# Kernel tuning notes

Measured on AMD Instinct MI355X. Metric: run time of the kernel, lower is better.

## Reference

```python
import jax, jax.numpy as jnp
import numpy as np

L, B, D = 512, 16, 256
H = 4            # MAX_DIFF == num_heads
MAX_BONDS = 6
MAX_DIFF = 4
PROB_SHIFT = 0.3


def _attn_weights(x, Wqk, Wq, bq, Wk, bk, mask):
    """Per-head softmax(QK^T/sqrt(hd)) with key padding mask.
    x: [b,l,d]; Wqk: [d,2d] (the inc/dec_qk pre-projection);
    Wq/Wk: [d,d] (MHA in_proj, stored x@W layout); mask: [b,l] bool (True=masked).
    Returns [b,h,l,l]. The V path / out_proj of the torch MHA are discarded
    by the original module, so they are omitted here.
    """
    b, l, d = x.shape
    hd = d // H
    q = x @ Wqk[:, :d]
    k = x @ Wqk[:, d:]
    Q = (q @ Wq + bq).reshape(b, l, H, hd)
    K = (k @ Wk + bk).reshape(b, l, H, hd)
    scores = jnp.einsum('blhd,bmhd->bhlm', Q, K) / np.sqrt(hd)
    scores = jnp.where(mask[:, None, None, :], -jnp.inf, scores)
    return jax.nn.softmax(scores, axis=-1)


def setup_inputs() -> dict:
    key = jax.random.key(0)
    ks = jax.random.split(key, 16)
    s = 0.05
    p = lambda k, shape: jax.random.normal(k, shape, jnp.float32) * s
    # key_padding_mask: last 64 positions padded (True == masked)
    src_mask = jnp.broadcast_to(jnp.arange(L)[None, :] >= (L - 64), (B, L))
    return {
        'molecule_embedding': jax.random.normal(ks[0], (L, B, D), jnp.float32),
        'src_bond': jax.random.randint(ks[1], (B, L, MAX_BONDS), 0, L, jnp.int32),
        'src_mask': src_mask,
        'W_inc_qk': p(ks[2], (D, 2 * D)),
        'Wq_inc': p(ks[3], (D, D)), 'bq_inc': p(ks[4], (D,)),
        'Wk_inc': p(ks[5], (D, D)), 'bk_inc': p(ks[6], (D,)),
        'W_dec_qk': p(ks[7], (D, 2 * D)),
        'Wq_dec': p(ks[8], (D, D)), 'bq_dec': p(ks[9], (D,)),
        'Wk_dec': p(ks[10], (D, D)), 'bk_dec': p(ks[11], (D,)),
        'Wc': p(ks[12], (MAX_DIFF, MAX_DIFF)), 'bc': p(ks[13], (MAX_DIFF,)),
    }


def reference(molecule_embedding, src_bond, src_mask,
              W_inc_qk, Wq_inc, bq_inc, Wk_inc, bk_inc,
              W_dec_qk, Wq_dec, bq_dec, Wk_dec, bk_dec,
              Wc, bc):
    x = jnp.transpose(molecule_embedding, (1, 0, 2))  # [b,l,d]
    b, l, _ = x.shape

    inc = _attn_weights(x, W_inc_qk, Wq_inc, bq_inc, Wk_inc, bk_inc, src_mask)
    dec = _attn_weights(x, W_dec_qk, Wq_dec, bq_dec, Wk_dec, bk_dec, src_mask)

    pad = (~src_mask).astype(jnp.float32)              # 1 - mask
    pm2 = pad[:, :, None] * pad[:, None, :]            # [b,l,l]

    # cls_layer((inc-dec).permute(0,2,3,1)) * (MAX_DIFF*pad_mask)[...,None]
    diff = (jnp.einsum('bhlm,hc->blmc', inc - dec, Wc) + bc)
    diff = diff * (MAX_DIFF * pm2)[..., None]          # [b,l,l,4]

    # src_bond has last dim == MAX_BONDS -> one-hot neighbor counts
    src_w = jax.nn.one_hot(src_bond, l, dtype=jnp.float32).sum(axis=2) * pm2  # [b,l,l]
    eye = jnp.eye(l, dtype=jnp.float32)
    src_w = src_w * (1.0 - eye)[None]                  # zero diagonal

    # _shift_probs(src_weight.long(), prob_shift, MAX_DIFF)
    oh = jax.nn.one_hot(src_w.astype(jnp.int32), MAX_DIFF, dtype=jnp.float32)
    probs = oh * (1.0 - PROB_SHIFT) + (1.0 - oh) * (PROB_SHIFT / (MAX_DIFF - 1))
    probs = probs / probs.sum(axis=-1, keepdims=True)

    return jnp.log(probs + 1e-6) + diff                # [b,l,l,4]
```

## Files before the change

kernel.cpp:

```cpp
#include <hip/hip_runtime.h>
#include <stdint.h>

typedef unsigned short u16t;
typedef short s8v __attribute__((ext_vector_type(8)));
typedef float f4v __attribute__((ext_vector_type(4)));

#define MFMA16 __builtin_amdgcn_mfma_f32_16x16x32_bf16
#define QKN (16*4*512*64)

__device__ __forceinline__ u16t f2bf(float f) {
  unsigned u = __builtin_bit_cast(unsigned, f);
  u += 0x7fffu + ((u >> 16) & 1u);
  return (u16t)(u >> 16);
}

__global__ __launch_bounds__(256) void prep_kernel(
    const float* __restrict__ Wiqk, const float* __restrict__ Wqi, const float* __restrict__ Wki,
    const float* __restrict__ Wdqk, const float* __restrict__ Wqd, const float* __restrict__ Wkd,
    u16t* __restrict__ weffT, const int* __restrict__ mraw, int* __restrict__ mdst) {
  __shared__ float At[16][65];
  __shared__ float Bt[16][65];
  __shared__ int mode;
  const int tid = threadIdx.x;

  if (blockIdx.z == 4) {
    if (tid == 0) mode = 0;
    __syncthreads();
    unsigned v0 = (unsigned)mraw[tid], v1 = (unsigned)mraw[tid + 256];
    if (v0 == 0x3F800000u || v1 == 0x3F800000u) mode = 2;
    __syncthreads();
    if (mode == 0 && (v0 > 1u || v1 > 1u)) mode = 1;
    __syncthreads();
    const int g = blockIdx.y * 4 + blockIdx.x;
#pragma unroll
    for (int i = 0; i < 2; ++i) {
      int idx = g * 512 + i * 256 + tid;
      int m;
      if (mode == 2)      m = (((const float*)mraw)[idx] != 0.0f) ? 1 : 0;
      else if (mode == 1) m = ((const unsigned char*)mraw)[idx];
      else                m = mraw[idx];
      mdst[idx] = m;
    }
    return;
  }

  const int n0 = blockIdx.x * 64;
  const int d0 = blockIdx.y * 64;
  const int p  = blockIdx.z;
  const float* A2  = (p == 0) ? Wqi : (p == 1) ? Wki : (p == 2) ? Wqd : Wkd;
  const float* Wqk = (p < 2) ? Wiqk : Wdqk;
  const int aoff = (p & 1) * 256;
  const int tx = tid & 15, ty = tid >> 4;

  float acc[4][4];
#pragma unroll
  for (int i = 0; i < 4; ++i)
#pragma unroll
    for (int j = 0; j < 4; ++j) acc[i][j] = 0.f;

  for (int k0 = 0; k0 < 256; k0 += 16) {
    __syncthreads();
    {
      int nn = tid & 63, kr = tid >> 6;
#pragma unroll
      for (int pass = 0; pass < 4; ++pass) {
        int kk = kr + pass * 4;
        At[kk][nn] = A2[(size_t)(k0 + kk) * 256 + n0 + nn];
      }
      int kk = tid & 15, dr = tid >> 4;
#pragma unroll
      for (int pass = 0; pass < 4; ++pass) {
        int dd = dr + pass * 16;
        Bt[kk][dd] = Wqk[(size_t)(d0 + dd) * 512 + aoff + k0 + kk];
      }
    }
    __syncthreads();
#pragma unroll
    for (int kk = 0; kk < 16; ++kk) {
      float a[4], b[4];
#pragma unroll
      for (int i = 0; i < 4; ++i) a[i] = At[kk][ty * 4 + i];
#pragma unroll
      for (int j = 0; j < 4; ++j) b[j] = Bt[kk][tx * 4 + j];
#pragma unroll
      for (int i = 0; i < 4; ++i)
#pragma unroll
        for (int j = 0; j < 4; ++j) acc[i][j] = fmaf(a[i], b[j], acc[i][j]);
    }
  }

#pragma unroll
  for (int i = 0; i < 4; ++i) {
    u16t h[4] = {f2bf(acc[i][0]), f2bf(acc[i][1]), f2bf(acc[i][2]), f2bf(acc[i][3])};
    *(uint2*)(&weffT[((size_t)(p * 256 + n0 + ty * 4 + i)) * 256 + d0 + tx * 4]) =
        *(const uint2*)h;
  }
}

__global__ __launch_bounds__(256) void proj_kernel(
    const float* __restrict__ emb, const u16t* __restrict__ weffT,
    const float* __restrict__ bq_inc, const float* __restrict__ bk_inc,
    const float* __restrict__ bq_dec, const float* __restrict__ bk_dec,
    u16t* __restrict__ qk) {
  __shared__ __align__(16) u16t As[128 * 40];
  __shared__ __align__(16) u16t Bs[128 * 40];
  const int t = threadIdx.x;
  const int n0 = blockIdx.x * 128;
  const int r0 = blockIdx.y * 128;
  const int bb = r0 >> 9;
  const int l0 = r0 & 511;
  const int lane = t & 63, wid = t >> 6;
  const int quad = lane >> 4, c15 = lane & 15;
  const int wm = wid >> 1, wn = wid & 1;

  f4v acc[4][4];
#pragma unroll
  for (int i = 0; i < 4; ++i)
#pragma unroll
    for (int j = 0; j < 4; ++j) acc[i][j] = f4v{0.f, 0.f, 0.f, 0.f};

  for (int k0 = 0; k0 < 256; k0 += 32) {
    __syncthreads();
#pragma unroll
    for (int i = 0; i < 2; ++i) {
      int c = t + i * 256;
      int m = c >> 2, off = (c & 3) * 8;
      const float* src = emb + (size_t)((l0 + m) * 16 + bb) * 256 + k0 + off;
      float4 x0 = *(const float4*)src;
      float4 x1 = *(const float4*)(src + 4);
      u16t h[8] = {f2bf(x0.x), f2bf(x0.y), f2bf(x0.z), f2bf(x0.w),
                   f2bf(x1.x), f2bf(x1.y), f2bf(x1.z), f2bf(x1.w)};
      *(uint4*)(&As[m * 40 + off]) = *(const uint4*)h;
      *(uint4*)(&Bs[m * 40 + off]) =
          *(const uint4*)(weffT + (size_t)(n0 + m) * 256 + k0 + off);
    }
    __syncthreads();
    s8v af[4], bf[4];
#pragma unroll
    for (int mi = 0; mi < 4; ++mi)
      af[mi] = *(const s8v*)(&As[(wm * 64 + mi * 16 + c15) * 40 + quad * 8]);
#pragma unroll
    for (int ni = 0; ni < 4; ++ni)
      bf[ni] = *(const s8v*)(&Bs[(wn * 64 + ni * 16 + c15) * 40 + quad * 8]);
#pragma unroll
    for (int mi = 0; mi < 4; ++mi)
#pragma unroll
      for (int ni = 0; ni < 4; ++ni)
        acc[mi][ni] = MFMA16(af[mi], bf[ni], acc[mi][ni], 0, 0, 0);
  }

  const float* biasP[4] = {bq_inc, bk_inc, bq_dec, bk_dec};
#pragma unroll
  for (int ni = 0; ni < 4; ++ni) {
    int n = n0 + wn * 64 + ni * 16 + c15;
    int p = n >> 8, h = (n >> 6) & 3, tt = n & 63, jj = n & 255;
    float bias = biasP[p][jj];
    u16t* dst = qk + (size_t)p * QKN;
#pragma unroll
    for (int mi = 0; mi < 4; ++mi) {
#pragma unroll
      for (int reg = 0; reg < 4; ++reg) {
        int l = l0 + wm * 64 + mi * 16 + quad * 4 + reg;
        dst[((size_t)(bb * 4 + h) * 512 + l) * 64 + tt] = f2bf(acc[mi][ni][reg] + bias);
      }
    }
  }
}

__global__ __launch_bounds__(512) void fused_kernel(
    const u16t* __restrict__ qk, const int* __restrict__ mask,
    const int* __restrict__ src_bond, const float* __restrict__ Wc,
    const float* __restrict__ bc, float* __restrict__ out) {
  __shared__ __align__(16) u16t Qs[8 * 16 * 72];
  __shared__ int bondsL[96];
  __shared__ int mlds[512 + 16];
  __shared__ float rpart[2][8][16];
  const int t = threadIdx.x;
  const int l0 = blockIdx.x * 16;
  const int bb = blockIdx.y;

#pragma unroll
  for (int i = 0; i < 2; ++i) {
    int c = t + i * 512;
    int q = c >> 7, row = (c >> 3) & 15, off = (c & 7) * 8;
    const u16t* Qb = qk + (size_t)(2 * (q >> 2)) * QKN;
    *(uint4*)(&Qs[(q * 16 + row) * 72 + off]) =
        *(const uint4*)(Qb + ((size_t)(bb * 4 + (q & 3)) * 512 + l0 + row) * 64 + off);
  }
  mlds[t] = mask[bb * 512 + t];
  if (t < 16) mlds[512 + t] = mask[bb * 512 + l0 + t];
  if (t < 96) bondsL[t] = src_bond[(size_t)(bb * 512 + l0 + t / 6) * 6 + (t % 6)];

  const int lane = t & 63, wid = t >> 6;
  const int quad = lane >> 4, c15 = lane & 15;

  float Wf[16];
#pragma unroll
  for (int i = 0; i < 16; ++i) Wf[i] = Wc[i];

  float dacc[4][4][4];
#pragma unroll
  for (int nt = 0; nt < 4; ++nt)
#pragma unroll
    for (int r = 0; r < 4; ++r)
#pragma unroll
      for (int c = 0; c < 4; ++c) dacc[nt][r][c] = 0.f;

  __syncthreads();

#pragma unroll 1
  for (int q = 0; q < 8; ++q) {
    const int pp = q >> 2, h = q & 3;
    const u16t* Kb = qk + (size_t)(2 * pp + 1) * QKN + (size_t)(bb * 4 + h) * 512 * 64;
    s8v a0 = *(const s8v*)(&Qs[(q * 16 + c15) * 72 + quad * 8]);
    s8v a1 = *(const s8v*)(&Qs[(q * 16 + c15) * 72 + 32 + quad * 8]);

    s8v kb0[4], kb1[4];
#pragma unroll
    for (int nt = 0; nt < 4; ++nt) {
      int m = wid * 64 + nt * 16 + c15;
      kb0[nt] = *(const s8v*)(Kb + (size_t)m * 64 + quad * 8);
      kb1[nt] = *(const s8v*)(Kb + (size_t)m * 64 + 32 + quad * 8);
    }

    float E[4][4];
    float rsum[4] = {0.f, 0.f, 0.f, 0.f};
#pragma unroll
    for (int nt = 0; nt < 4; ++nt) {
      f4v sacc = f4v{0.f, 0.f, 0.f, 0.f};
      sacc = MFMA16(a0, kb0[nt], sacc, 0, 0, 0);
      sacc = MFMA16(a1, kb1[nt], sacc, 0, 0, 0);
      int m = wid * 64 + nt * 16 + c15;
      bool msk = (mlds[m] != 0);
#pragma unroll
      for (int reg = 0; reg < 4; ++reg) {
        float e = msk ? 0.f : __expf(sacc[reg] * 0.125f);
        E[nt][reg] = e;
        rsum[reg] += e;
      }
    }

#pragma unroll
    for (int reg = 0; reg < 4; ++reg) {
#pragma unroll
      for (int off = 1; off < 16; off <<= 1) rsum[reg] += __shfl_xor(rsum[reg], off);
    }
    if (c15 == 0) {
#pragma unroll
      for (int reg = 0; reg < 4; ++reg) rpart[q & 1][wid][quad * 4 + reg] = rsum[reg];
    }
    __syncthreads();

    float inv[4];
    const float sgn = pp ? -1.f : 1.f;
#pragma unroll
    for (int reg = 0; reg < 4; ++reg) {
      float tot = 0.f;
#pragma unroll
      for (int w = 0; w < 8; ++w) tot += rpart[q & 1][w][quad * 4 + reg];
      inv[reg] = sgn / tot;
    }

#pragma unroll
    for (int nt = 0; nt < 4; ++nt) {
#pragma unroll
      for (int reg = 0; reg < 4; ++reg) {
        float P = E[nt][reg] * inv[reg];
#pragma unroll
        for (int c = 0; c < 4; ++c)
          dacc[nt][reg][c] = fmaf(P, Wf[h * 4 + c], dacc[nt][reg][c]);
      }
    }
  }

  float bcF[4];
#pragma unroll
  for (int c = 0; c < 4; ++c) bcF[c] = bc[c];
  const float lgH = logf(0.7f + 1e-6f);
  const float lgM = logf(0.1f + 1e-6f);
  const float lgU = logf(0.25f + 1e-6f);

#pragma unroll
  for (int nt = 0; nt < 4; ++nt) {
    int m = wid * 64 + nt * 16 + c15;
    bool padm = (mlds[m] == 0);
#pragma unroll
    for (int reg = 0; reg < 4; ++reg) {
      int lloc = quad * 4 + reg;
      int l = l0 + lloc;
      bool padl = (mlds[512 + lloc] == 0);
      bool pm = padl && padm;
      int cnt = 0;
#pragma unroll
      for (int j = 0; j < 6; ++j) cnt += (bondsL[lloc * 6 + j] == m) ? 1 : 0;
      int cls = (pm && (m != l)) ? cnt : 0;
      float v[4];
#pragma unroll
      for (int c = 0; c < 4; ++c) {
        float lp = (cls >= 4) ? lgU : ((c == cls) ? lgH : lgM);
        float dv = pm ? 4.f * (dacc[nt][reg][c] + bcF[c]) : 0.f;
        v[c] = lp + dv;
      }
      float4 o = make_float4(v[0], v[1], v[2], v[3]);
      *(float4*)(&out[((size_t)(bb * 512 + l) * 512 + m) * 4]) = o;
    }
  }
}

extern "C" void kernel_launch(void* const* d_in, const int* in_sizes, int n_in,
                              void* d_out, int out_size, void* d_ws, size_t ws_size,
                              hipStream_t stream) {
  (void)in_sizes; (void)n_in; (void)out_size; (void)ws_size;
  const float* emb      = (const float*)d_in[0];
  const int*   src_bond = (const int*)d_in[1];
  const int*   mask_raw = (const int*)d_in[2];
  const float* W_inc_qk = (const float*)d_in[3];
  const float* Wq_inc   = (const float*)d_in[4];
  const float* bq_inc   = (const float*)d_in[5];
  const float* Wk_inc   = (const float*)d_in[6];
  const float* bk_inc   = (const float*)d_in[7];
  const float* W_dec_qk = (const float*)d_in[8];
  const float* Wq_dec   = (const float*)d_in[9];
  const float* bq_dec   = (const float*)d_in[10];
  const float* Wk_dec   = (const float*)d_in[11];
  const float* bk_dec   = (const float*)d_in[12];
  const float* Wc       = (const float*)d_in[13];
  const float* bc       = (const float*)d_in[14];
  float* out = (float*)d_out;

  char* ws = (char*)d_ws;
  int*   wsMask = (int*)ws;
  u16t*  weffT  = (u16t*)(ws + 32768);
  u16t*  qk     = (u16t*)(ws + 32768 + 524288);

  hipLaunchKernelGGL(prep_kernel, dim3(4, 4, 5), dim3(256), 0, stream,
                     W_inc_qk, Wq_inc, Wk_inc, W_dec_qk, Wq_dec, Wk_dec, weffT,
                     mask_raw, wsMask);
  hipLaunchKernelGGL(proj_kernel, dim3(8, 64), dim3(256), 0, stream,
                     emb, weffT, bq_inc, bk_inc, bq_dec, bk_dec, qk);
  hipLaunchKernelGGL(fused_kernel, dim3(32, 16), dim3(512), 0, stream,
                     qk, wsMask, src_bond, Wc, bc, out);
}
```

Before: 195.2 us.

## Prefetch next head's K tiles, remap blocks across batches, move Wc to LDS

The K fragments for the next head are loaded into registers while the current head's softmax reduction and accumulation run, so global load latency overlaps with compute instead of stalling each iteration. Block indices are remapped so that neighbouring workgroups cover different batches, which spreads K reads across batches and XCDs. Wc is staged through LDS rather than held as 16 registers, the key mask is hoisted out of the loop, and the partial-sum layout is transposed so each row total is read with two float4 loads. The prefetch raises register pressure because K is live across the barrier, and the block remap assumes a 32x16 grid.

```diff
diff --git a/kernel.cpp b/kernel.cpp
--- a/kernel.cpp
+++ b/kernel.cpp
@@ -174,10 +174,14 @@
   __shared__ __align__(16) u16t Qs[8 * 16 * 72];
   __shared__ int bondsL[96];
   __shared__ int mlds[512 + 16];
-  __shared__ float rpart[2][8][16];
+  __shared__ __align__(16) float rpart[2][16][8];
+  __shared__ float wlds[16];
   const int t = threadIdx.x;
-  const int l0 = blockIdx.x * 16;
-  const int bb = blockIdx.y;
+
+  const int f = (int)(blockIdx.x + gridDim.x * blockIdx.y);
+  const int j = f >> 3;
+  const int bb = (f & 7) * 2 + (j >> 5);
+  const int l0 = (j & 31) * 16;
 
 #pragma unroll
   for (int i = 0; i < 2; ++i) {
@@ -190,13 +194,11 @@
   mlds[t] = mask[bb * 512 + t];
   if (t < 16) mlds[512 + t] = mask[bb * 512 + l0 + t];
   if (t < 96) bondsL[t] = src_bond[(size_t)(bb * 512 + l0 + t / 6) * 6 + (t % 6)];
+  if (t >= 96 && t < 112) wlds[t - 96] = Wc[t - 96];
 
   const int lane = t & 63, wid = t >> 6;
   const int quad = lane >> 4, c15 = lane & 15;
-
-  float Wf[16];
-#pragma unroll
-  for (int i = 0; i < 16; ++i) Wf[i] = Wc[i];
+  const int mbase = wid * 64 + c15;
 
   float dacc[4][4][4];
 #pragma unroll
@@ -206,22 +208,32 @@
 #pragma unroll
       for (int c = 0; c < 4; ++c) dacc[nt][r][c] = 0.f;
 
+  s8v kb0[4], kb1[4];
+  {
+    const u16t* Kb = qk + (size_t)1 * QKN + (size_t)(bb * 4 + 0) * 512 * 64;
+#pragma unroll
+    for (int nt = 0; nt < 4; ++nt) {
+      const u16t* row = Kb + (size_t)(mbase + nt * 16) * 64 + quad * 8;
+      kb0[nt] = *(const s8v*)row;
+      kb1[nt] = *(const s8v*)(row + 32);
+    }
+  }
+
   __syncthreads();
+
+  bool mskm[4];
+#pragma unroll
+  for (int nt = 0; nt < 4; ++nt) mskm[nt] = (mlds[mbase + nt * 16] != 0);
 
 #pragma unroll 1
   for (int q = 0; q < 8; ++q) {
     const int pp = q >> 2, h = q & 3;
-    const u16t* Kb = qk + (size_t)(2 * pp + 1) * QKN + (size_t)(bb * 4 + h) * 512 * 64;
     s8v a0 = *(const s8v*)(&Qs[(q * 16 + c15) * 72 + quad * 8]);
     s8v a1 = *(const s8v*)(&Qs[(q * 16 + c15) * 72 + 32 + quad * 8]);
 
-    s8v kb0[4], kb1[4];
-#pragma unroll
-    for (int nt = 0; nt < 4; ++nt) {
-      int m = wid * 64 + nt * 16 + c15;
-      kb0[nt] = *(const s8v*)(Kb + (size_t)m * 64 + quad * 8);
-      kb1[nt] = *(const s8v*)(Kb + (size_t)m * 64 + 32 + quad * 8);
-    }
+    float wv[4];
+#pragma unroll
+    for (int c = 0; c < 4; ++c) wv[c] = wlds[h * 4 + c];
 
     float E[4][4];
     float rsum[4] = {0.f, 0.f, 0.f, 0.f};
@@ -230,16 +242,26 @@
       f4v sacc = f4v{0.f, 0.f, 0.f, 0.f};
       sacc = MFMA16(a0, kb0[nt], sacc, 0, 0, 0);
       sacc = MFMA16(a1, kb1[nt], sacc, 0, 0, 0);
-      int m = wid * 64 + nt * 16 + c15;
-      bool msk = (mlds[m] != 0);
 #pragma unroll
       for (int reg = 0; reg < 4; ++reg) {
-        float e = msk ? 0.f : __expf(sacc[reg] * 0.125f);
+        float e = mskm[nt] ? 0.f : __expf(sacc[reg] * 0.125f);
         E[nt][reg] = e;
         rsum[reg] += e;
       }
     }
 
+    if (q < 7) {
+      const int qn = q + 1;
+      const u16t* Kb = qk + (size_t)(2 * (qn >> 2) + 1) * QKN
+                          + (size_t)(bb * 4 + (qn & 3)) * 512 * 64;
+#pragma unroll
+      for (int nt = 0; nt < 4; ++nt) {
+        const u16t* row = Kb + (size_t)(mbase + nt * 16) * 64 + quad * 8;
+        kb0[nt] = *(const s8v*)row;
+        kb1[nt] = *(const s8v*)(row + 32);
+      }
+    }
+
 #pragma unroll
     for (int reg = 0; reg < 4; ++reg) {
 #pragma unroll
@@ -247,7 +269,7 @@
     }
     if (c15 == 0) {
 #pragma unroll
-      for (int reg = 0; reg < 4; ++reg) rpart[q & 1][wid][quad * 4 + reg] = rsum[reg];
+      for (int reg = 0; reg < 4; ++reg) rpart[q & 1][quad * 4 + reg][wid] = rsum[reg];
     }
     __syncthreads();
 
@@ -255,10 +277,9 @@
     const float sgn = pp ? -1.f : 1.f;
 #pragma unroll
     for (int reg = 0; reg < 4; ++reg) {
-      float tot = 0.f;
-#pragma unroll
-      for (int w = 0; w < 8; ++w) tot += rpart[q & 1][w][quad * 4 + reg];
-      inv[reg] = sgn / tot;
+      const float4* rp = (const float4*)&rpart[q & 1][quad * 4 + reg][0];
+      float4 s0 = rp[0], s1 = rp[1];
+      inv[reg] = sgn / (s0.x + s0.y + s0.z + s0.w + s1.x + s1.y + s1.z + s1.w);
     }
 
 #pragma unroll
@@ -268,7 +289,7 @@
         float P = E[nt][reg] * inv[reg];
 #pragma unroll
         for (int c = 0; c < 4; ++c)
-          dacc[nt][reg][c] = fmaf(P, Wf[h * 4 + c], dacc[nt][reg][c]);
+          dacc[nt][reg][c] = fmaf(P, wv[c], dacc[nt][reg][c]);
       }
     }
   }
@@ -282,8 +303,8 @@
 
 #pragma unroll
   for (int nt = 0; nt < 4; ++nt) {
-    int m = wid * 64 + nt * 16 + c15;
-    bool padm = (mlds[m] == 0);
+    int m = mbase + nt * 16;
+    bool padm = !mskm[nt];
 #pragma unroll
     for (int reg = 0; reg < 4; ++reg) {
       int lloc = quad * 4 + reg;
@@ -292,7 +313,7 @@
       bool pm = padl && padm;
       int cnt = 0;
 #pragma unroll
-      for (int j = 0; j < 6; ++j) cnt += (bondsL[lloc * 6 + j] == m) ? 1 : 0;
+      for (int j6 = 0; j6 < 6; ++j6) cnt += (bondsL[lloc * 6 + j6] == m) ? 1 : 0;
       int cls = (pm && (m != l)) ? cnt : 0;
       float v[4];
 #pragma unroll
```

After: 175.1 us. 1.11x faster.
